# Performance work log

Measured on AMD Instinct MI355X. Metric: run time of the kernel, lower is better.

## Reference

```python
import jax, jax.numpy as jnp
import numpy as np

BLOCK_SIZE = 64
N_EMBD = 128
N_HEAD = 4
HEAD_DIM = N_EMBD // N_HEAD  # 32


def setup_inputs() -> dict:
    key = jax.random.key(0)
    kx, kq, kk, kv = jax.random.split(key, 4)
    B, T = 4096, 64
    x = jax.random.normal(kx, (B, T, N_EMBD), dtype=jnp.float32)
    # nn.Linear(n_embd, head_dim, bias=False): stored as [out,in] in torch,
    # here kept as [in, out] = [128, 32] so projection is x @ W.
    s = 1.0 / np.sqrt(N_EMBD)
    Wq = jax.random.uniform(kq, (N_EMBD, HEAD_DIM), jnp.float32, -s, s)
    Wk = jax.random.uniform(kk, (N_EMBD, HEAD_DIM), jnp.float32, -s, s)
    Wv = jax.random.uniform(kv, (N_EMBD, HEAD_DIM), jnp.float32, -s, s)
    return {"x": x, "Wq": Wq, "Wk": Wk, "Wv": Wv}


def reference(x, Wq, Wk, Wv):
    B, T, C = x.shape
    q = x @ Wq  # [B, T, Hd]
    k = x @ Wk
    v = x @ Wv
    scale = 1.0 / jnp.sqrt(jnp.asarray(k.shape[-1], x.dtype))
    wei = jnp.einsum("btd,bsd->bts", q, k) * scale  # [B, T, T]
    causal = jnp.tril(jnp.ones((T, T), dtype=bool))
    wei = jnp.where(causal, wei, -jnp.inf)
    wei = jax.nn.softmax(wei, axis=-1)
    out = jnp.einsum("bts,bsd->btd", wei, v)  # [B, T, Hd]
    return out
```

## Files before the change

### kernel.cpp

```cpp
#include <hip/hip_runtime.h>


#define TT 64
#define CC 128
#define HD 32

typedef __bf16 bf16_t;
typedef __bf16 bf8_t __attribute__((ext_vector_type(8)));
typedef __bf16 bf4_t __attribute__((ext_vector_type(4)));
typedef float  f4_t  __attribute__((ext_vector_type(4)));

__global__ __launch_bounds__(256) void prep_weights(
    const float* __restrict__ Wq, const float* __restrict__ Wk,
    const float* __restrict__ Wv, bf16_t* __restrict__ wf)
{
  int t = blockIdx.x * 256 + threadIdx.x;
  int j    = t & 7;
  int lane = (t >> 3) & 63;
  int kt   = (t >> 9) & 3;
  int n6   = t >> 11;
  int k    = kt * 32 + (lane >> 4) * 8 + j;
  int col  = (n6 & 1) * 16 + (lane & 15);
  const float* W = (n6 >> 1) == 0 ? Wq : ((n6 >> 1) == 1 ? Wk : Wv);
  float v = W[k * HD + col];
  if (n6 < 2) v *= 0.17677669529663687f;
  wf[t] = (bf16_t)v;
}

__global__ __launch_bounds__(64, 2) void head_fused(
    const float* __restrict__ x, const bf8_t* __restrict__ wf,
    float* __restrict__ out)
{
  __shared__ __align__(16) bf16_t qs[TT][40];
  __shared__ __align__(16) bf16_t ks[TT][40];
  __shared__ __align__(16) bf16_t vt[HD][72];
  __shared__ __align__(16) bf16_t ps[16][72];

  const int lane = threadIdx.x;
  const int quad = lane >> 4;
  const int l16  = lane & 15;
  const int b    = blockIdx.x;
  const float* __restrict__ xblk = x + (size_t)b * (TT * CC);
  float* __restrict__ ob = out + (size_t)b * (TT * HD);

  const f4_t zero4 = {0.f, 0.f, 0.f, 0.f};

  bf8_t wfr[24];

  auto load_tile = [&](float4* d, int i) {
    #pragma unroll
    for (int kk = 0; kk < 4; ++kk) {
      const float* s = xblk + (16 * i + l16) * CC + kk * 32 + quad * 8;
      d[2 * kk]     = *(const float4*)s;
      d[2 * kk + 1] = *(const float4*)(s + 4);
    }
  };

  auto proj_tile = [&](const float4* d, int i) {
    f4_t acc[6];
    #pragma unroll
    for (int n = 0; n < 6; ++n) acc[n] = zero4;
    #pragma unroll
    for (int kk = 0; kk < 4; ++kk) {
      float4 f0 = d[2 * kk], f1 = d[2 * kk + 1];
      bf8_t a;
      a[0] = (bf16_t)f0.x; a[1] = (bf16_t)f0.y; a[2] = (bf16_t)f0.z; a[3] = (bf16_t)f0.w;
      a[4] = (bf16_t)f1.x; a[5] = (bf16_t)f1.y; a[6] = (bf16_t)f1.z; a[7] = (bf16_t)f1.w;
      #pragma unroll
      for (int n = 0; n < 6; ++n)
        acc[n] = __builtin_amdgcn_mfma_f32_16x16x32_bf16(a, wfr[n * 4 + kk], acc[n], 0, 0, 0);
    }
    #pragma unroll
    for (int r = 0; r < 4; ++r) {
      int row = 16 * i + quad * 4 + r;
      qs[row][l16]      = (bf16_t)acc[0][r];
      qs[row][16 + l16] = (bf16_t)acc[1][r];
      ks[row][l16]      = (bf16_t)acc[2][r];
      ks[row][16 + l16] = (bf16_t)acc[3][r];
    }
    bf4_t v0 = { (bf16_t)acc[4][0], (bf16_t)acc[4][1], (bf16_t)acc[4][2], (bf16_t)acc[4][3] };
    bf4_t v1 = { (bf16_t)acc[5][0], (bf16_t)acc[5][1], (bf16_t)acc[5][2], (bf16_t)acc[5][3] };
    *(bf4_t*)&vt[l16][16 * i + quad * 4]      = v0;
    *(bf4_t*)&vt[16 + l16][16 * i + quad * 4] = v1;
  };

  float4 ta[8], tb[8];
  load_tile(ta, 0);
  #pragma unroll
  for (int t = 0; t < 24; ++t) wfr[t] = wf[t * 64 + lane];
  load_tile(tb, 1);
  proj_tile(ta, 0);
  load_tile(ta, 2);
  proj_tile(tb, 1);
  load_tile(tb, 3);
  proj_tile(ta, 2);
  proj_tile(tb, 3);

  #pragma unroll
  for (int i = 0; i < 4; ++i) {
    f4_t sc[4];
    bf8_t aq = *(const bf8_t*)&qs[16 * i + l16][quad * 8];
    #pragma unroll
    for (int j = 0; j < 4; ++j) {
      sc[j] = zero4;
      if (j <= i) {
        bf8_t bk = *(const bf8_t*)&ks[16 * j + l16][quad * 8];
        sc[j] = __builtin_amdgcn_mfma_f32_16x16x32_bf16(aq, bk, zero4, 0, 0, 0);
      }
    }
    #pragma unroll
    for (int r = 0; r < 4; ++r) {
      int rl = quad * 4 + r;
      float p[4];
      float psum = 0.f;
      #pragma unroll
      for (int j = 0; j < 4; ++j) {
        if (j <= i) {
          bool valid = (j < i) | (l16 <= rl);
          float e = __expf(sc[j][r]);
          p[j] = valid ? e : 0.f;
          psum += p[j];
        } else p[j] = 0.f;
      }
      #pragma unroll
      for (int off = 1; off < 16; off <<= 1)
        psum += __shfl_xor(psum, off);
      float inv = __builtin_amdgcn_rcpf(psum);
      #pragma unroll
      for (int j = 0; j < 4; ++j) {
        if (j <= i)             ps[rl][j * 16 + l16] = (bf16_t)(p[j] * inv);
        else if (j == (i | 1))  ps[rl][j * 16 + l16] = (bf16_t)0.f;
      }
    }
    f4_t o0 = zero4, o1 = zero4;
    #pragma unroll
    for (int kk = 0; kk <= (i >> 1); ++kk) {
      int k0 = kk * 32 + quad * 8;
      bf8_t ap  = *(const bf8_t*)&ps[l16][k0];
      bf8_t bv0 = *(const bf8_t*)&vt[l16][k0];
      bf8_t bv1 = *(const bf8_t*)&vt[16 + l16][k0];
      o0 = __builtin_amdgcn_mfma_f32_16x16x32_bf16(ap, bv0, o0, 0, 0, 0);
      o1 = __builtin_amdgcn_mfma_f32_16x16x32_bf16(ap, bv1, o1, 0, 0, 0);
    }
    #pragma unroll
    for (int r = 0; r < 4; ++r) {
      int row = 16 * i + quad * 4 + r;
      ob[row * HD + l16]      = o0[r];
      ob[row * HD + 16 + l16] = o1[r];
    }
  }
}

extern "C" void kernel_launch(void* const* d_in, const int* in_sizes, int n_in,
                              void* d_out, int out_size, void* d_ws, size_t ws_size,
                              hipStream_t stream) {
  const float* x  = (const float*)d_in[0];
  const float* Wq = (const float*)d_in[1];
  const float* Wk = (const float*)d_in[2];
  const float* Wv = (const float*)d_in[3];
  float* out = (float*)d_out;
  bf16_t* wf = (bf16_t*)d_ws;
  int B = in_sizes[0] / (TT * CC);

  prep_weights<<<dim3(48), dim3(256), 0, stream>>>(Wq, Wk, Wv, wf);
  head_fused<<<dim3(B), dim3(64), 0, stream>>>(x, (const bf8_t*)wf, out);
}
```

Baseline: 209.5 us.

## Process two batches per block and compute softmax row sums with MFMA

Each 64-thread block now handles two batch elements. It prefetches the second batch's x tiles while the first batch's attention phase runs, and the projection weights held in registers are reused across both. The softmax no longer normalises through a cross-lane shuffle reduction. Unnormalised exponentials are written to LDS, the row sums come from an extra MFMA against a vector of ones, and the outputs are divided at the end. The cost is half as many blocks and more live registers. The row sums are also taken from bf16-rounded exponentials, which slightly changes the numerics.

```diff
diff --git a/kernel.cpp b/kernel.cpp
--- a/kernel.cpp
+++ b/kernel.cpp
@@ -39,18 +39,20 @@
   const int lane = threadIdx.x;
   const int quad = lane >> 4;
   const int l16  = lane & 15;
-  const int b    = blockIdx.x;
-  const float* __restrict__ xblk = x + (size_t)b * (TT * CC);
-  float* __restrict__ ob = out + (size_t)b * (TT * HD);
+  const size_t b0 = (size_t)blockIdx.x * 2;
+  const float* __restrict__ xb[2] = { x + b0 * (TT * CC), x + (b0 + 1) * (TT * CC) };
+  float* __restrict__ ob[2] = { out + b0 * (TT * HD), out + (b0 + 1) * (TT * HD) };
 
   const f4_t zero4 = {0.f, 0.f, 0.f, 0.f};
+  const bf8_t ones = { (bf16_t)1.f, (bf16_t)1.f, (bf16_t)1.f, (bf16_t)1.f,
+                       (bf16_t)1.f, (bf16_t)1.f, (bf16_t)1.f, (bf16_t)1.f };
 
   bf8_t wfr[24];
 
-  auto load_tile = [&](float4* d, int i) {
+  auto load_tile = [&](float4* d, int bb, int i) {
     #pragma unroll
     for (int kk = 0; kk < 4; ++kk) {
-      const float* s = xblk + (16 * i + l16) * CC + kk * 32 + quad * 8;
+      const float* s = xb[bb] + (16 * i + l16) * CC + kk * 32 + quad * 8;
       d[2 * kk]     = *(const float4*)s;
       d[2 * kk + 1] = *(const float4*)(s + 4);
     }
@@ -84,71 +86,75 @@
     *(bf4_t*)&vt[16 + l16][16 * i + quad * 4] = v1;
   };
 
+  auto phase2 = [&](float* obase) {
+    #pragma unroll
+    for (int i = 0; i < 4; ++i) {
+      f4_t sc[4];
+      bf8_t aq = *(const bf8_t*)&qs[16 * i + l16][quad * 8];
+      #pragma unroll
+      for (int j = 0; j < 4; ++j) {
+        sc[j] = zero4;
+        if (j <= i) {
+          bf8_t bk = *(const bf8_t*)&ks[16 * j + l16][quad * 8];
+          sc[j] = __builtin_amdgcn_mfma_f32_16x16x32_bf16(aq, bk, zero4, 0, 0, 0);
+        }
+      }
+      #pragma unroll
+      for (int r = 0; r < 4; ++r) {
+        int rl = quad * 4 + r;
+        #pragma unroll
+        for (int j = 0; j < 4; ++j) {
+          if (j <= i) {
+            bool valid = (j < i) | (l16 <= rl);
+            float e = valid ? __expf(sc[j][r]) : 0.f;
+            ps[rl][j * 16 + l16] = (bf16_t)e;
+          } else if (j == (i | 1)) {
+            ps[rl][j * 16 + l16] = (bf16_t)0.f;
+          }
+        }
+      }
+      f4_t o0 = zero4, o1 = zero4, rs = zero4;
+      #pragma unroll
+      for (int kk = 0; kk <= (i >> 1); ++kk) {
+        int k0 = kk * 32 + quad * 8;
+        bf8_t ap  = *(const bf8_t*)&ps[l16][k0];
+        bf8_t bv0 = *(const bf8_t*)&vt[l16][k0];
+        bf8_t bv1 = *(const bf8_t*)&vt[16 + l16][k0];
+        o0 = __builtin_amdgcn_mfma_f32_16x16x32_bf16(ap, bv0, o0, 0, 0, 0);
+        o1 = __builtin_amdgcn_mfma_f32_16x16x32_bf16(ap, bv1, o1, 0, 0, 0);
+        rs = __builtin_amdgcn_mfma_f32_16x16x32_bf16(ap, ones, rs, 0, 0, 0);
+      }
+      #pragma unroll
+      for (int r = 0; r < 4; ++r) {
+        float inv = __builtin_amdgcn_rcpf(rs[r]);
+        int row = 16 * i + quad * 4 + r;
+        obase[row * HD + l16]      = o0[r] * inv;
+        obase[row * HD + 16 + l16] = o1[r] * inv;
+      }
+    }
+  };
+
   float4 ta[8], tb[8];
-  load_tile(ta, 0);
+  load_tile(ta, 0, 0);
   #pragma unroll
   for (int t = 0; t < 24; ++t) wfr[t] = wf[t * 64 + lane];
-  load_tile(tb, 1);
+  load_tile(tb, 0, 1);
   proj_tile(ta, 0);
-  load_tile(ta, 2);
+  load_tile(ta, 0, 2);
   proj_tile(tb, 1);
-  load_tile(tb, 3);
+  load_tile(tb, 0, 3);
+  proj_tile(ta, 2);
+  load_tile(ta, 1, 0);
+  proj_tile(tb, 3);
+  load_tile(tb, 1, 1);
+  phase2(ob[0]);
+  proj_tile(ta, 0);
+  load_tile(ta, 1, 2);
+  proj_tile(tb, 1);
+  load_tile(tb, 1, 3);
   proj_tile(ta, 2);
   proj_tile(tb, 3);
-
-  #pragma unroll
-  for (int i = 0; i < 4; ++i) {
-    f4_t sc[4];
-    bf8_t aq = *(const bf8_t*)&qs[16 * i + l16][quad * 8];
-    #pragma unroll
-    for (int j = 0; j < 4; ++j) {
-      sc[j] = zero4;
-      if (j <= i) {
-        bf8_t bk = *(const bf8_t*)&ks[16 * j + l16][quad * 8];
-        sc[j] = __builtin_amdgcn_mfma_f32_16x16x32_bf16(aq, bk, zero4, 0, 0, 0);
-      }
-    }
-    #pragma unroll
-    for (int r = 0; r < 4; ++r) {
-      int rl = quad * 4 + r;
-      float p[4];
-      float psum = 0.f;
-      #pragma unroll
-      for (int j = 0; j < 4; ++j) {
-        if (j <= i) {
-          bool valid = (j < i) | (l16 <= rl);
-          float e = __expf(sc[j][r]);
-          p[j] = valid ? e : 0.f;
-          psum += p[j];
-        } else p[j] = 0.f;
-      }
-      #pragma unroll
-      for (int off = 1; off < 16; off <<= 1)
-        psum += __shfl_xor(psum, off);
-      float inv = __builtin_amdgcn_rcpf(psum);
-      #pragma unroll
-      for (int j = 0; j < 4; ++j) {
-        if (j <= i)             ps[rl][j * 16 + l16] = (bf16_t)(p[j] * inv);
-        else if (j == (i | 1))  ps[rl][j * 16 + l16] = (bf16_t)0.f;
-      }
-    }
-    f4_t o0 = zero4, o1 = zero4;
-    #pragma unroll
-    for (int kk = 0; kk <= (i >> 1); ++kk) {
-      int k0 = kk * 32 + quad * 8;
-      bf8_t ap  = *(const bf8_t*)&ps[l16][k0];
-      bf8_t bv0 = *(const bf8_t*)&vt[l16][k0];
-      bf8_t bv1 = *(const bf8_t*)&vt[16 + l16][k0];
-      o0 = __builtin_amdgcn_mfma_f32_16x16x32_bf16(ap, bv0, o0, 0, 0, 0);
-      o1 = __builtin_amdgcn_mfma_f32_16x16x32_bf16(ap, bv1, o1, 0, 0, 0);
-    }
-    #pragma unroll
-    for (int r = 0; r < 4; ++r) {
-      int row = 16 * i + quad * 4 + r;
-      ob[row * HD + l16]      = o0[r];
-      ob[row * HD + 16 + l16] = o1[r];
-    }
-  }
+  phase2(ob[1]);
 }
 
 extern "C" void kernel_launch(void* const* d_in, const int* in_sizes, int n_in,
@@ -161,7 +167,8 @@
   float* out = (float*)d_out;
   bf16_t* wf = (bf16_t*)d_ws;
   int B = in_sizes[0] / (TT * CC);
+  int nblk = B / 2;
 
   prep_weights<<<dim3(48), dim3(256), 0, stream>>>(Wq, Wk, Wv, wf);
-  head_fused<<<dim3(B), dim3(64), 0, stream>>>(x, (const bf8_t*)wf, out);
+  head_fused<<<dim3(nblk), dim3(64), 0, stream>>>(x, (const bf8_t*)wf, out);
 }
```

Result: slower. 213.8 us (+2.0%).
